# Kernel optimization log

Hardware: AMD Instinct MI355X
Metric: run time of the kernel (lower is better)

The kernel has to match this reference:

```python
import jax, jax.numpy as jnp
import numpy as np

DN = ('NCHW', 'OIHW', 'NCHW')

def conv3x3(x, w, b):
    y = jax.lax.conv_general_dilated(x, w, window_strides=(1, 1), padding='SAME', dimension_numbers=DN)
    return y + b[None, :, None, None]

def setup_inputs() -> dict:
    key = jax.random.key(0)
    ks = jax.random.split(key, 12)
    B, C, H, W, r = 4, 64, 128, 128, 2
    ic = C * r * r  # 256
    s = 0.02
    inp = {
        'x': jax.random.normal(ks[0], (B, C, H, W), jnp.float32),
        'g_w': jax.random.normal(ks[1], (ic, ic), jnp.float32) * s,
        'g_b': jnp.zeros((ic,), jnp.float32),
        'theta_w': jax.random.normal(ks[2], (ic, ic), jnp.float32) * s,
        'theta_b': jnp.zeros((ic,), jnp.float32),
        'phi_w': jax.random.normal(ks[3], (ic, ic), jnp.float32) * s,
        'phi_b': jnp.zeros((ic,), jnp.float32),
        'Ws_w': jax.random.normal(ks[4], (C, C), jnp.float32) * s,
        'Ws_b': jnp.zeros((C,), jnp.float32),
        'Wc_w': jax.random.normal(ks[5], (C, C), jnp.float32) * s,
        'Wc_b': jnp.zeros((C,), jnp.float32),
        'gamma_s': jnp.ones((1,), jnp.float32),
        'gamma_c': jnp.ones((1,), jnp.float32),
        'm1_w': jax.random.normal(ks[6], (16, C, 3, 3), jnp.float32) * s,
        'm1_b': jnp.zeros((16,), jnp.float32),
        'm2_w': jax.random.normal(ks[7], (1, 16, 3, 3), jnp.float32) * s,
        'm2_b': jnp.zeros((1,), jnp.float32),
    }
    return inp

def reference(x, g_w, g_b, theta_w, theta_b, phi_w, phi_b, Ws_w, Ws_b, Wc_w, Wc_b, gamma_s, gamma_c, m1_w, m1_b, m2_w, m2_b):
    b, c, h, w = x.shape
    ic = g_w.shape[0]
    r = int(round((ic // c) ** 0.5))
    hr, wr = h // r, w // r
    n = hr * wr  # spatial positions after channel-folding
    # x1: [b, ic, n] (row-major reshape, same as torch .reshape)
    x1 = x.reshape(b, ic, n)
    # 1x1 convs == channel matmuls
    g_x = jnp.einsum('oi,bin->bno', g_w, x1) + g_b          # [b, n, ic]
    th = jnp.einsum('oi,bin->bon', theta_w, x1) + theta_b[:, None]  # [b, ic, n]
    ph = jnp.einsum('oi,bin->bon', phi_w, x1) + phi_b[:, None]      # [b, ic, n]
    # spatial attention: [b, n, n]
    f_s = jnp.einsum('bcn,bcm->bnm', th, ph)
    f_s = jax.nn.softmax(f_s, axis=-1)
    y_s = jnp.einsum('bnm,bmo->bno', f_s, g_x)              # [b, n, ic]
    y_s = jnp.transpose(y_s, (0, 2, 1)).reshape(b, c, h, w)
    # channel attention: [b, ic, ic]
    f_c = jnp.einsum('bcn,bdn->bcd', th, ph)
    f_c = jax.nn.softmax(f_c, axis=-1)
    y_c = jnp.einsum('bno,bod->bnd', g_x, f_c).reshape(b, c, h, w)
    ws = jnp.einsum('oi,bihw->bohw', Ws_w, y_s) + Ws_b[None, :, None, None]
    wc = jnp.einsum('oi,bihw->bohw', Wc_w, y_c) + Wc_b[None, :, None, None]
    z = x + gamma_s[0] * ws + gamma_c[0] * wc
    hmid = jax.nn.relu(conv3x3(z, m1_w, m1_b))
    logit = conv3x3(hmid, m2_w, m2_b)
    return (logit, z)
```

## Files before the change

### kernel.cpp

```cpp
#include <hip/hip_runtime.h>
#include <stdint.h>

typedef unsigned short u16;
typedef unsigned int   u32;

typedef __attribute__((ext_vector_type(8)))  short bf16x8;
typedef __attribute__((ext_vector_type(4)))  float f32x4;
typedef __attribute__((ext_vector_type(4)))  unsigned int u32x4;

__device__ __forceinline__ float b2f(u16 u) { return __uint_as_float(((u32)u) << 16); }
__device__ __forceinline__ float blo(u32 u) { return __uint_as_float(u << 16); }
__device__ __forceinline__ float bhi(u32 u) { return __uint_as_float(u & 0xffff0000u); }
__device__ __forceinline__ u16 f2b(float f) {
    u32 x = __float_as_uint(f);
    u32 r = (x + 0x7fffu + ((x >> 16) & 1u)) >> 16;
    return (u16)r;
}

#define NB   4
#define IC   256
#define NPOS 4096
#define CH   64
#define HW   16384

__global__ __launch_bounds__(256) void prep_kernel(
    const float* __restrict__ wsw, const float* __restrict__ wcw,
    const float* __restrict__ m1w,
    const float* __restrict__ thw, const float* __restrict__ phw, const float* __restrict__ gw,
    float* __restrict__ wswT, float* __restrict__ wcwT, float* __restrict__ m1wT,
    u16* __restrict__ wbf)
{
    int idx = blockIdx.x * 256 + threadIdx.x;
    if (idx < 65536) {
        wbf[idx]          = f2b(thw[idx]);
        wbf[idx + 65536]  = f2b(phw[idx]);
        wbf[idx + 131072] = f2b(gw[idx]);
    }
    if (idx < 4096) {
        int i = idx >> 6, c = idx & 63;
        wswT[i*64 + c] = wsw[c*64 + i];
        wcwT[i*64 + c] = wcw[c*64 + i];
    }
    if (idx < 9216) {
        int o = idx & 15, ct = idx >> 4;
        int t = ct % 9, c = ct / 9;
        m1wT[idx] = m1w[(o*64 + c)*9 + t];
    }
}

__global__ __launch_bounds__(256) void qkv_mfma_kernel(
    const float* __restrict__ x, const u16* __restrict__ wbf,
    const float* __restrict__ thb, const float* __restrict__ phb, const float* __restrict__ gb,
    u16* __restrict__ Q, u16* __restrict__ K, u16* __restrict__ VT)
{
    __shared__ __align__(16) u32 xT[64*132];
    __shared__ __align__(16) float bias_l[256];
    const int tid  = threadIdx.x;
    const int w    = tid >> 6;
    const int lane = tid & 63;
    const int q4   = lane >> 4;
    const int l    = lane & 15;
    const int n0   = blockIdx.x * 64;
    const int b    = blockIdx.y;
    const int mat  = blockIdx.z;
    const u16* wmat = wbf + mat * 65536;
    const float* bias = (mat == 0) ? thb : (mat == 1) ? phb : gb;

    bias_l[tid] = bias[tid];

    {
        const float* xb = x + ((size_t)b*IC)*NPOS + n0;
        int n   = tid & 63;
        int ip0 = tid >> 6;
        #pragma unroll 4
        for (int p=0; p<32; p++){
            int ip = ip0 + p*4;
            float v0 = xb[(size_t)(2*ip  )*NPOS + n];
            float v1 = xb[(size_t)(2*ip+1)*NPOS + n];
            xT[n*132 + ip] = (u32)f2b(v0) | ((u32)f2b(v1) << 16);
        }
    }
    __syncthreads();

    f32x4 acc[4][4];
    #pragma unroll
    for (int ot=0; ot<4; ot++)
        #pragma unroll
        for (int nt=0; nt<4; nt++) acc[ot][nt] = (f32x4){0.f,0.f,0.f,0.f};

    #pragma unroll
    for (int f=0; f<8; f++){
        bf16x8 bfrag[4];
        #pragma unroll
        for (int nt=0; nt<4; nt++)
            bfrag[nt] = *(const bf16x8*)&xT[(nt*16 + l)*132 + f*16 + q4*4];
        #pragma unroll
        for (int ot=0; ot<4; ot++){
            bf16x8 afrag = *(const bf16x8*)(wmat + (size_t)(w*64 + ot*16 + l)*256 + f*32 + q4*8);
            #pragma unroll
            for (int nt=0; nt<4; nt++)
                acc[ot][nt] = __builtin_amdgcn_mfma_f32_16x16x32_bf16(afrag, bfrag[nt], acc[ot][nt], 0, 0, 0);
        }
    }
    __syncthreads();

    if (mat < 2){
        u16* zbuf = (u16*)xT;
        #pragma unroll
        for (int nt=0; nt<4; nt++)
            #pragma unroll
            for (int ot=0; ot<4; ot++){
                int o = w*64 + ot*16 + q4*4;
                float4 bv = *(const float4*)&bias_l[o];
                uint2 pk;
                pk.x = (u32)f2b(acc[ot][nt][0]+bv.x) | ((u32)f2b(acc[ot][nt][1]+bv.y) << 16);
                pk.y = (u32)f2b(acc[ot][nt][2]+bv.z) | ((u32)f2b(acc[ot][nt][3]+bv.w) << 16);
                *(uint2*)&zbuf[(nt*16 + l)*264 + o] = pk;
            }
        __syncthreads();
        u16* dst = ((mat == 0) ? Q : K) + ((size_t)(b*NPOS + n0))*IC;
        int n = tid >> 2, o0 = (tid & 3)*64;
        const u32* src = &xT[n*132 + (tid & 3)*32];
        #pragma unroll
        for (int m=0; m<8; m++)
            *(uint4*)(dst + (size_t)n*IC + o0 + m*8) = ((const uint4*)src)[m];
    } else {
        u16* zbuf = (u16*)xT;
        #pragma unroll
        for (int nt=0; nt<4; nt++)
            #pragma unroll
            for (int ot=0; ot<4; ot++){
                int o = w*64 + ot*16 + q4*4;
                int n = nt*16 + l;
                #pragma unroll
                for (int reg=0; reg<4; reg++)
                    zbuf[(o+reg)*66 + n] = f2b(acc[ot][nt][reg] + bias_l[o+reg]);
            }
        __syncthreads();
        const u32* src = &xT[tid*33];
        u32 tmp[32];
        #pragma unroll
        for (int m=0; m<32; m++) tmp[m] = src[m];
        u16* dst = VT + ((size_t)(b*IC + tid))*NPOS + n0;
        #pragma unroll
        for (int m=0; m<8; m++){
            uint4 v; v.x = tmp[m*4]; v.y = tmp[m*4+1]; v.z = tmp[m*4+2]; v.w = tmp[m*4+3];
            *(uint4*)(dst + m*8) = v;
        }
    }
}

__global__ __launch_bounds__(256) void fc_mfma_kernel(
    const u16* __restrict__ Q, const u16* __restrict__ K, float* __restrict__ fcp)
{
    __shared__ __align__(16) u16 QT[64*72];
    __shared__ __align__(16) u16 KT[64*72];
    const int tid = threadIdx.x;
    const int w   = tid >> 6;
    const int lane = tid & 63;
    const int q4  = lane >> 4;
    const int l   = lane & 15;
    const int c0  = blockIdx.x * 64;
    const int d0  = blockIdx.y * 64;
    const int b   = blockIdx.z >> 2;
    const int nseg= blockIdx.z & 3;

    f32x4 acc[4];
    #pragma unroll
    for (int dt=0; dt<4; dt++) acc[dt] = (f32x4){0.f,0.f,0.f,0.f};

    for (int chunk=0; chunk<16; chunk++){
        const int n0 = nseg*1024 + chunk*64;
        __syncthreads();
        {
            int r  = tid >> 2;
            int cq = (tid & 3) * 16;
            const u16* qs = Q + ((size_t)(b*NPOS + n0 + r))*IC + c0 + cq;
            const u16* ks = K + ((size_t)(b*NPOS + n0 + r))*IC + d0 + cq;
            u16 qv[16], kv[16];
            *(uint4*)&qv[0] = *(const uint4*)qs;
            *(uint4*)&qv[8] = *(const uint4*)(qs + 8);
            *(uint4*)&kv[0] = *(const uint4*)ks;
            *(uint4*)&kv[8] = *(const uint4*)(ks + 8);
            #pragma unroll
            for (int j=0;j<16;j++){
                QT[(cq+j)*72 + r] = qv[j];
                KT[(cq+j)*72 + r] = kv[j];
            }
        }
        __syncthreads();
        #pragma unroll
        for (int f=0; f<2; f++){
            bf16x8 af = *(const bf16x8*)&QT[(w*16 + l)*72 + f*32 + q4*8];
            #pragma unroll
            for (int dt=0; dt<4; dt++){
                bf16x8 bf2 = *(const bf16x8*)&KT[(dt*16 + l)*72 + f*32 + q4*8];
                acc[dt] = __builtin_amdgcn_mfma_f32_16x16x32_bf16(af, bf2, acc[dt], 0, 0, 0);
            }
        }
    }

    #pragma unroll
    for (int dt=0; dt<4; dt++)
        #pragma unroll
        for (int reg=0; reg<4; reg++)
            fcp[((size_t)((nseg*NB + b)*256 + c0 + w*16 + q4*4 + reg))*256 + d0 + dt*16 + l] = acc[dt][reg];
}

__global__ __launch_bounds__(256) void softmax_fc_kernel(
    const float* __restrict__ fcp, float* __restrict__ pc)
{
    __shared__ float red[8];
    const int tid = threadIdx.x;
    const int b = blockIdx.x >> 8, c = blockIdx.x & 255;
    float v = 0.f;
    #pragma unroll
    for (int s=0; s<4; s++)
        v += fcp[((size_t)((s*NB + b)*256 + c))*256 + tid];
    float m = v;
    #pragma unroll
    for (int d=32; d>=1; d>>=1) m = fmaxf(m, __shfl_xor(m, d));
    if ((tid & 63) == 0) red[tid>>6] = m;
    __syncthreads();
    m = fmaxf(fmaxf(red[0],red[1]), fmaxf(red[2],red[3]));
    float e = __expf(v - m);
    float s = e;
    #pragma unroll
    for (int d=32; d>=1; d>>=1) s += __shfl_xor(s, d);
    if ((tid & 63) == 0) red[4 + (tid>>6)] = s;
    __syncthreads();
    s = red[4]+red[5]+red[6]+red[7];
    pc[(size_t)b*65536 + (size_t)c*256 + tid] = e / s;
}

__global__ __launch_bounds__(256) void yc_kernel(
    const u16* __restrict__ VT, const float* __restrict__ pc, u16* __restrict__ ycb)
{
    __shared__ __align__(16) u16 Vt_l[32*64];
    __shared__ __align__(16) float Pt[32*64];
    const int tid = threadIdx.x;
    const int n0 = blockIdx.x * 64, d0 = blockIdx.y * 64, b = blockIdx.z;
    const int tn = tid >> 4, td = tid & 15;
    float acc[4][4];
    #pragma unroll
    for (int j=0;j<4;j++)
        #pragma unroll
        for (int d=0;d<4;d++) acc[j][d]=0.f;
    for (int ot=0; ot<8; ot++){
        int o0 = ot*32;
        __syncthreads();
        {
            int ol = tid >> 3, cc = tid & 7;
            *(uint4*)&Vt_l[ol*64 + cc*8] = *(const uint4*)(VT + ((size_t)(b*IC + o0 + ol))*NPOS + n0 + cc*8);
            const float* ps = pc + (size_t)b*65536 + (size_t)(o0 + ol)*256 + d0 + cc*8;
            *(float4*)&Pt[ol*64 + cc*8]     = *(const float4*)ps;
            *(float4*)&Pt[ol*64 + cc*8 + 4] = *(const float4*)(ps + 4);
        }
        __syncthreads();
        #pragma unroll 4
        for (int kk=0; kk<32; kk++){
            float4 pv = *(const float4*)&Pt[kk*64 + td*4];
            uint2 vp = *(const uint2*)&Vt_l[kk*64 + tn*4];
            float v0 = blo(vp.x), v1 = bhi(vp.x), v2 = blo(vp.y), v3 = bhi(vp.y);
            acc[0][0] = fmaf(v0, pv.x, acc[0][0]); acc[0][1] = fmaf(v0, pv.y, acc[0][1]);
            acc[0][2] = fmaf(v0, pv.z, acc[0][2]); acc[0][3] = fmaf(v0, pv.w, acc[0][3]);
            acc[1][0] = fmaf(v1, pv.x, acc[1][0]); acc[1][1] = fmaf(v1, pv.y, acc[1][1]);
            acc[1][2] = fmaf(v1, pv.z, acc[1][2]); acc[1][3] = fmaf(v1, pv.w, acc[1][3]);
            acc[2][0] = fmaf(v2, pv.x, acc[2][0]); acc[2][1] = fmaf(v2, pv.y, acc[2][1]);
            acc[2][2] = fmaf(v2, pv.z, acc[2][2]); acc[2][3] = fmaf(v2, pv.w, acc[2][3]);
            acc[3][0] = fmaf(v3, pv.x, acc[3][0]); acc[3][1] = fmaf(v3, pv.y, acc[3][1]);
            acc[3][2] = fmaf(v3, pv.z, acc[3][2]); acc[3][3] = fmaf(v3, pv.w, acc[3][3]);
        }
    }
    #pragma unroll
    for (int j=0;j<4;j++){
        u32 lo = (u32)f2b(acc[j][0]) | ((u32)f2b(acc[j][1]) << 16);
        u32 hi = (u32)f2b(acc[j][2]) | ((u32)f2b(acc[j][3]) << 16);
        *(uint2*)&ycb[((size_t)b*NPOS + n0 + tn*4 + j)*IC + d0 + td*4] = make_uint2(lo,hi);
    }
}

__global__ __launch_bounds__(256) void flash_mfma_kernel(
    const u16* __restrict__ Q, const u16* __restrict__ K, const u16* __restrict__ VT,
    u16* __restrict__ opart0, u16* __restrict__ opartx, float* __restrict__ lpart,
    int sshift)
{
    __shared__ __align__(16) u32 Kt[8192];
    __shared__ __align__(16) u32 Vt[8192];
    __shared__ __align__(16) u16 Pl[4608];
    const int tid  = threadIdx.x;
    const int w    = tid >> 6;
    const int lane = tid & 63;
    const int q4   = lane >> 4;
    const int l    = lane & 15;
    const int S    = 1 << sshift;

    const int id   = blockIdx.x;
    const int xcd  = id & 7;
    const int b    = xcd >> 1;
    const int h    = xcd & 1;
    const int r    = id >> 3;
    const int n0   = ((r & 31) | (h << 5)) * 64;
    const int seg  = r >> 5;
    const int tiles = 64 >> sshift;
    const int kt0   = seg * tiles;

    bf16x8 qf[8];
    {
        const u16* qrow = Q + ((size_t)(b*NPOS + n0 + w*16 + l))*IC;
        #pragma unroll
        for (int f=0; f<8; f++){
            u32x4 qv = __builtin_nontemporal_load((const u32x4*)(qrow + f*32 + q4*8));
            qf[f] = *(bf16x8*)&qv;
        }
    }

    f32x4 oacc[16];
    #pragma unroll
    for (int t=0;t<16;t++) oacc[t] = (f32x4){0.f,0.f,0.f,0.f};
    float lrow[4] = {0.f, 0.f, 0.f, 0.f};

    u16* Pz = Pl + w*1152;

    auto stage_k = [&](int m0s){
        #pragma unroll
        for (int j=0;j<8;j++){
            int call = w*8 + j;
            int rr = call*2 + (lane>>5);
            int c = (lane & 31) ^ (rr & 7);
            const u16* g = K + ((size_t)(b*NPOS + m0s + rr))*IC + c*8;
            __builtin_amdgcn_global_load_lds(
                (const __attribute__((address_space(1))) u32*)(const void*)g,
                (__attribute__((address_space(3))) u32*)(void*)&Kt[call*256], 16, 0, 0);
        }
    };
    auto stage_v = [&](int m0s){
        #pragma unroll
        for (int j=0;j<8;j++){
            int call = w*8 + j;
            int d = call*8 + (lane>>3);
            int c = (lane & 7) ^ (d & 7);
            const u16* g = VT + ((size_t)(b*IC + d))*NPOS + m0s + c*8;
            __builtin_amdgcn_global_load_lds(
                (const __attribute__((address_space(1))) u32*)(const void*)g,
                (__attribute__((address_space(3))) u32*)(void*)&Vt[call*256], 16, 0, 0);
        }
    };

    stage_k(kt0*64);
    stage_v(kt0*64);
    asm volatile("s_waitcnt vmcnt(0)" ::: "memory");
    __builtin_amdgcn_sched_barrier(0);
    __builtin_amdgcn_s_barrier();
    __builtin_amdgcn_sched_barrier(0);

    for (int kti=0; kti<tiles; kti++){
        const bool more = (kti + 1 < tiles);
        const int mn = (kt0 + kti + 1)*64;

        f32x4 sac[4];
        #pragma unroll
        for (int t=0;t<4;t++) sac[t] = (f32x4){0.f,0.f,0.f,0.f};
        __builtin_amdgcn_s_setprio(1);
        #pragma unroll
        for (int f=0; f<8; f++){
            #pragma unroll
            for (int t=0;t<4;t++){
                int rr = t*16 + l;
                int c = (f*4 + q4) ^ (rr & 7);
                bf16x8 kf = *(const bf16x8*)((const u16*)Kt + rr*256 + c*8);
                sac[t] = __builtin_amdgcn_mfma_f32_16x16x32_bf16(qf[f], kf, sac[t], 0, 0, 0);
            }
        }
        __builtin_amdgcn_s_setprio(0);

        __builtin_amdgcn_sched_barrier(0);
        __builtin_amdgcn_s_barrier();
        __builtin_amdgcn_sched_barrier(0);

        if (more) stage_k(mn);

        #pragma unroll
        for (int reg=0; reg<4; reg++){
            float p0 = __expf(sac[0][reg]), p1 = __expf(sac[1][reg]);
            float p2 = __expf(sac[2][reg]), p3 = __expf(sac[3][reg]);
            lrow[reg] += (p0+p1) + (p2+p3);
            int m = q4*4 + reg;
            Pz[m*72 + l]      = f2b(p0);
            Pz[m*72 + 16 + l] = f2b(p1);
            Pz[m*72 + 32 + l] = f2b(p2);
            Pz[m*72 + 48 + l] = f2b(p3);
        }

        if (more) { asm volatile("s_waitcnt vmcnt(8)" ::: "memory"); }
        else      { asm volatile("s_waitcnt vmcnt(0)" ::: "memory"); }
        __builtin_amdgcn_sched_barrier(0);
        __builtin_amdgcn_s_barrier();
        __builtin_amdgcn_sched_barrier(0);

        __builtin_amdgcn_s_setprio(1);
        #pragma unroll
        for (int s2=0; s2<2; s2++){
            bf16x8 pa = *(const bf16x8*)(Pz + l*72 + s2*32 + q4*8);
            #pragma unroll
            for (int t=0;t<16;t++){
                int d = t*16 + l;
                int c = (s2*4 + q4) ^ (d & 7);
                bf16x8 vb = *(const bf16x8*)((const u16*)Vt + d*64 + c*8);
                oacc[t] = __builtin_amdgcn_mfma_f32_16x16x32_bf16(pa, vb, oacc[t], 0, 0, 0);
            }
        }
        __builtin_amdgcn_s_setprio(0);

        __builtin_amdgcn_sched_barrier(0);
        __builtin_amdgcn_s_barrier();
        __builtin_amdgcn_sched_barrier(0);

        if (more) {
            stage_v(mn);
            asm volatile("s_waitcnt vmcnt(8)" ::: "memory");
        } else {
            asm volatile("s_waitcnt vmcnt(0)" ::: "memory");
        }
        __builtin_amdgcn_sched_barrier(0);
        __builtin_amdgcn_s_barrier();
        __builtin_amdgcn_sched_barrier(0);
    }

    #pragma unroll
    for (int reg=0; reg<4; reg++){
        float v = lrow[reg];
        v += __shfl_xor(v, 1); v += __shfl_xor(v, 2);
        v += __shfl_xor(v, 4); v += __shfl_xor(v, 8);
        if (l == 0)
            lpart[((size_t)(seg*NB + b))*NPOS + n0 + w*16 + q4*4 + reg] = v;
    }

    __syncthreads();
    u16* Ez = (u16*)Kt + w*4096;
    #pragma unroll
    for (int t=0;t<16;t++)
        #pragma unroll
        for (int reg=0;reg<4;reg++)
            Ez[(t*16 + l)*16 + q4*4 + reg] = f2b(oacc[t][reg]);
    u16* base = (seg == 0) ? opart0 : (opartx + (size_t)(seg-1)*((size_t)NB*IC*NPOS));
    u16* dst = base + (size_t)b*(IC*NPOS) + n0 + w*16;
    for (int p=0; p<32; p++){
        int d = p*8 + (lane>>3);
        u32 val = *(const u32*)(Ez + d*16 + (lane&7)*2);
        __builtin_nontemporal_store(val, (u32*)(dst + (size_t)d*NPOS + (lane&7)*2));
    }
}

__global__ __launch_bounds__(256) void combine_kernel(
    u16* __restrict__ opart0, const u16* __restrict__ opartx,
    const float* __restrict__ lpart, int S)
{
    const int idx = blockIdx.x * 256 + threadIdx.x;
    const int b   = idx >> 17;
    const int rem = idx & 131071;
    const int o   = rem >> 9;
    const int n   = (rem & 511) * 8;
    const size_t base = ((size_t)b*IC + o)*NPOS + n;
    float acc[8] = {0,0,0,0,0,0,0,0};
    float L[8]   = {0,0,0,0,0,0,0,0};
    for (int s=0; s<S; s++){
        const u16* p = (s == 0) ? opart0 : (opartx + (size_t)(s-1)*((size_t)NB*IC*NPOS));
        uint4 v = *(const uint4*)(p + base);
        acc[0] += blo(v.x); acc[1] += bhi(v.x);
        acc[2] += blo(v.y); acc[3] += bhi(v.y);
        acc[4] += blo(v.z); acc[5] += bhi(v.z);
        acc[6] += blo(v.w); acc[7] += bhi(v.w);
        const float* lp = lpart + ((size_t)(s*NB + b))*NPOS + n;
        float4 l0 = *(const float4*)lp;
        float4 l1 = *(const float4*)(lp + 4);
        L[0]+=l0.x; L[1]+=l0.y; L[2]+=l0.z; L[3]+=l0.w;
        L[4]+=l1.x; L[5]+=l1.y; L[6]+=l1.z; L[7]+=l1.w;
    }
    uint4 out;
    out.x = (u32)f2b(acc[0]/L[0]) | ((u32)f2b(acc[1]/L[1]) << 16);
    out.y = (u32)f2b(acc[2]/L[2]) | ((u32)f2b(acc[3]/L[3]) << 16);
    out.z = (u32)f2b(acc[4]/L[4]) | ((u32)f2b(acc[5]/L[5]) << 16);
    out.w = (u32)f2b(acc[6]/L[6]) | ((u32)f2b(acc[7]/L[7]) << 16);
    *(uint4*)(opart0 + base) = out;
}

__global__ __launch_bounds__(256) void z_kernel(
    const float* __restrict__ x, const u16* __restrict__ ysT, const u16* __restrict__ ycb,
    const float* __restrict__ wswT, const float* __restrict__ wcwT,
    const float* __restrict__ wsb, const float* __restrict__ wcb,
    const float* __restrict__ gs, const float* __restrict__ gc,
    float* __restrict__ zout)
{
    __shared__ __align__(16) float Wsl[64*32];
    __shared__ __align__(16) float Wcl[64*32];
    const int tid = threadIdx.x;
    const int p = blockIdx.x * 256 + tid;
    const int cbase = blockIdx.y * 32;
    const int b = blockIdx.z;
    {
        int i = tid >> 2, c8 = (tid & 3) * 8;
        const float* s1 = wswT + i*64 + cbase + c8;
        const float* s2 = wcwT + i*64 + cbase + c8;
        *(float4*)&Wsl[i*32 + c8]     = *(const float4*)s1;
        *(float4*)&Wsl[i*32 + c8 + 4] = *(const float4*)(s1+4);
        *(float4*)&Wcl[i*32 + c8]     = *(const float4*)s2;
        *(float4*)&Wcl[i*32 + c8 + 4] = *(const float4*)(s2+4);
    }
    __syncthreads();
    float as[32], ac[32];
    #pragma unroll
    for (int c=0;c<32;c++){ as[c]=0.f; ac[c]=0.f; }
    const u16* ysp = ysT + (size_t)b*(IC*NPOS) + p;
    const u16* ycp = ycb + (size_t)b*(IC*NPOS) + p;
    for (int i=0;i<64;i++){
        float ysv = b2f(ysp[(size_t)i*HW]);
        float ycv = b2f(ycp[(size_t)i*HW]);
        #pragma unroll
        for (int c=0;c<32;c++){
            as[c] = fmaf(Wsl[i*32+c], ysv, as[c]);
            ac[c] = fmaf(Wcl[i*32+c], ycv, ac[c]);
        }
    }
    float gsv = gs[0], gcv = gc[0];
    #pragma unroll
    for (int c=0;c<32;c++){
        int cg = cbase + c;
        float xv = x[((size_t)b*CH + cg)*HW + p];
        float zv = fmaf(gsv, as[c] + wsb[cg], xv);
        zv = fmaf(gcv, ac[c] + wcb[cg], zv);
        zout[((size_t)b*CH + cg)*HW + p] = zv;
    }
}

__global__ __launch_bounds__(256) void conv1_kernel(
    const float* __restrict__ z, const float* __restrict__ m1wT, const float* __restrict__ m1b,
    float* __restrict__ hmid)
{
    const int tid = threadIdx.x;
    const int p = blockIdx.x * 128 + (tid & 127);
    const int oh = (tid >> 7) * 8;
    const int b = blockIdx.y;
    const int y = p >> 7, xx = p & 127;
    float acc[8];
    #pragma unroll
    for (int o=0;o<8;o++) acc[o]=0.f;
    for (int c=0;c<64;c++){
        const float* zp = z + ((size_t)b*CH + c)*HW;
        #pragma unroll
        for (int t=0;t<9;t++){
            int dy = t/3 - 1, dx = t%3 - 1;
            int yy = y + dy, xv = xx + dx;
            float zv = 0.f;
            if (yy >= 0 && yy < 128 && xv >= 0 && xv < 128) zv = zp[yy*128 + xv];
            const float* w = m1wT + (c*9 + t)*16 + oh;
            #pragma unroll
            for (int o=0;o<8;o++) acc[o] = fmaf(w[o], zv, acc[o]);
        }
    }
    #pragma unroll
    for (int o=0;o<8;o++)
        hmid[((size_t)b*16 + oh + o)*HW + p] = fmaxf(acc[o] + m1b[oh + o], 0.f);
}

__global__ __launch_bounds__(256) void conv2_kernel(
    const float* __restrict__ hmid, const float* __restrict__ m2w, const float* __restrict__ m2b,
    float* __restrict__ logit)
{
    const int idx = blockIdx.x * 256 + threadIdx.x;
    const int b = idx >> 14, p = idx & 16383;
    const int y = p >> 7, xx = p & 127;
    float acc = 0.f;
    for (int c=0;c<16;c++){
        const float* hp = hmid + ((size_t)b*16 + c)*HW;
        #pragma unroll
        for (int t=0;t<9;t++){
            int dy = t/3 - 1, dx = t%3 - 1;
            int yy = y + dy, xv = xx + dx;
            if (yy >= 0 && yy < 128 && xv >= 0 && xv < 128)
                acc = fmaf(m2w[c*9+t], hp[yy*128 + xv], acc);
        }
    }
    logit[idx] = acc + m2b[0];
}

extern "C" void kernel_launch(void* const* d_in, const int* in_sizes, int n_in,
                              void* d_out, int out_size, void* d_ws, size_t ws_size,
                              hipStream_t stream)
{
    const float* x    = (const float*)d_in[0];
    const float* g_w  = (const float*)d_in[1];
    const float* g_b  = (const float*)d_in[2];
    const float* th_w = (const float*)d_in[3];
    const float* th_b = (const float*)d_in[4];
    const float* ph_w = (const float*)d_in[5];
    const float* ph_b = (const float*)d_in[6];
    const float* ws_w = (const float*)d_in[7];
    const float* ws_b = (const float*)d_in[8];
    const float* wc_w = (const float*)d_in[9];
    const float* wc_b = (const float*)d_in[10];
    const float* gs   = (const float*)d_in[11];
    const float* gc   = (const float*)d_in[12];
    const float* m1w  = (const float*)d_in[13];
    const float* m1b  = (const float*)d_in[14];
    const float* m2w  = (const float*)d_in[15];
    const float* m2b  = (const float*)d_in[16];

    char* ws = (char*)d_ws;
    u16*   Qb   = (u16*)  (ws + 0);
    u16*   Kb   = (u16*)  (ws + 8388608);
    u16*   VTb  = (u16*)  (ws + 16777216);
    u16*   ysT  = (u16*)  (ws + 25165824);
    u16*   ycb  = (u16*)  (ws + 33554432);
    u16*   wbf  = (u16*)  (ws + 41943040);
    float* pc   = (float*)(ws + 42991616);
    float* fcp  = (float*)(ws + 44040192);
    float* hmid = (float*)(ws + 44040192);
    float* lpart= (float*)(ws + 44040192);
    float* wswT = (float*)(ws + 48234496);
    float* wcwT = (float*)(ws + 48250880);
    float* m1wT = (float*)(ws + 48267264);
    u16*   opartx = (u16*)(ws + 48304128);

    float* logit = (float*)d_out;
    float* zout  = (float*)d_out + 65536;

    int sshift = 0;
    if (ws_size >= 48304128ULL + 3ULL*8388608ULL)      sshift = 2;
    else if (ws_size >= 48304128ULL + 1ULL*8388608ULL) sshift = 1;

    prep_kernel<<<256, 256, 0, stream>>>(ws_w, wc_w, m1w, th_w, ph_w, g_w,
                                         wswT, wcwT, m1wT, wbf);
    qkv_mfma_kernel<<<dim3(64,4,3), 256, 0, stream>>>(x, wbf, th_b, ph_b, g_b, Qb, Kb, VTb);
    fc_mfma_kernel<<<dim3(4,4,16), 256, 0, stream>>>(Qb, Kb, fcp);
    softmax_fc_kernel<<<1024, 256, 0, stream>>>(fcp, pc);
    yc_kernel<<<dim3(64,4,4), 256, 0, stream>>>(VTb, pc, ycb);
    flash_mfma_kernel<<<dim3(NB * 64 * (1 << sshift)), 256, 0, stream>>>(Qb, Kb, VTb, ysT, opartx, lpart, sshift);
    combine_kernel<<<2048, 256, 0, stream>>>(ysT, opartx, lpart, 1 << sshift);
    z_kernel<<<dim3(64,2,4), 256, 0, stream>>>(x, ysT, ycb, wswT, wcwT, ws_b, wc_b, gs, gc, zout);
    conv1_kernel<<<dim3(128,4), 256, 0, stream>>>(zout, m1wT, m1b, hmid);
    conv2_kernel<<<256, 256, 0, stream>>>(hmid, m2w, m2b, logit);
}
```

Baseline: 459.2 us.

## Split flash attention warps into 2x2 query-key/dim grid to reuse fragments

Each of the four warps now owns 32 query rows and half of the key columns (for QK) or half of the head dimension (for PV), instead of 16 query rows over the full tile. Each K and V fragment loaded from LDS now feeds two MFMAs, which halves LDS read traffic per MFMA. The P buffer uses a new XOR swizzle, and row sums are combined across the two key-half warps through LDS at the end. The cost is more query-fragment registers and an extra barrier plus reduction in the epilogue.

```diff
diff --git a/kernel.cpp b/kernel.cpp
--- a/kernel.cpp
+++ b/kernel.cpp
@@ -287,12 +287,14 @@
 {
     __shared__ __align__(16) u32 Kt[8192];
     __shared__ __align__(16) u32 Vt[8192];
-    __shared__ __align__(16) u16 Pl[4608];
+    __shared__ __align__(16) u16 Pl[4096];
     const int tid  = threadIdx.x;
     const int w    = tid >> 6;
     const int lane = tid & 63;
     const int q4   = lane >> 4;
     const int l    = lane & 15;
+    const int wq   = w >> 1;
+    const int wk   = w & 1;
     const int S    = 1 << sshift;
 
     const int id   = blockIdx.x;
@@ -305,22 +307,26 @@
     const int tiles = 64 >> sshift;
     const int kt0   = seg * tiles;
 
-    bf16x8 qf[8];
+    bf16x8 qf[2][8];
     {
-        const u16* qrow = Q + ((size_t)(b*NPOS + n0 + w*16 + l))*IC;
-        #pragma unroll
-        for (int f=0; f<8; f++){
-            u32x4 qv = __builtin_nontemporal_load((const u32x4*)(qrow + f*32 + q4*8));
-            qf[f] = *(bf16x8*)&qv;
-        }
-    }
-
-    f32x4 oacc[16];
-    #pragma unroll
-    for (int t=0;t<16;t++) oacc[t] = (f32x4){0.f,0.f,0.f,0.f};
-    float lrow[4] = {0.f, 0.f, 0.f, 0.f};
-
-    u16* Pz = Pl + w*1152;
+        const u16* qbase = Q + ((size_t)(b*NPOS + n0 + wq*32 + l))*IC;
+        #pragma unroll
+        for (int qt=0; qt<2; qt++)
+            #pragma unroll
+            for (int f=0; f<8; f++){
+                u32x4 qv = __builtin_nontemporal_load((const u32x4*)(qbase + qt*16*IC + f*32 + q4*8));
+                qf[qt][f] = *(bf16x8*)&qv;
+            }
+    }
+
+    f32x4 oacc[2][8];
+    #pragma unroll
+    for (int qt=0; qt<2; qt++)
+        #pragma unroll
+        for (int dt=0; dt<8; dt++) oacc[qt][dt] = (f32x4){0.f,0.f,0.f,0.f};
+    float lrow[2][4] = {{0.f,0.f,0.f,0.f},{0.f,0.f,0.f,0.f}};
+
+    u16* Pz = Pl + wq*2048;
 
     auto stage_k = [&](int m0s){
         #pragma unroll
@@ -358,18 +364,21 @@
         const bool more = (kti + 1 < tiles);
         const int mn = (kt0 + kti + 1)*64;
 
-        f32x4 sac[4];
-        #pragma unroll
-        for (int t=0;t<4;t++) sac[t] = (f32x4){0.f,0.f,0.f,0.f};
+        f32x4 sac[2][2];
+        #pragma unroll
+        for (int qt=0; qt<2; qt++)
+            #pragma unroll
+            for (int kt2=0; kt2<2; kt2++) sac[qt][kt2] = (f32x4){0.f,0.f,0.f,0.f};
         __builtin_amdgcn_s_setprio(1);
         #pragma unroll
         for (int f=0; f<8; f++){
-            #pragma unroll
-            for (int t=0;t<4;t++){
-                int rr = t*16 + l;
-                int c = (f*4 + q4) ^ (rr & 7);
-                bf16x8 kf = *(const bf16x8*)((const u16*)Kt + rr*256 + c*8);
-                sac[t] = __builtin_amdgcn_mfma_f32_16x16x32_bf16(qf[f], kf, sac[t], 0, 0, 0);
+            int c = (f*4 + q4) ^ (l & 7);
+            bf16x8 kf0 = *(const bf16x8*)((const u16*)Kt + (wk*32 + l)*256 + c*8);
+            bf16x8 kf1 = *(const bf16x8*)((const u16*)Kt + (wk*32 + 16 + l)*256 + c*8);
+            #pragma unroll
+            for (int qt=0; qt<2; qt++){
+                sac[qt][0] = __builtin_amdgcn_mfma_f32_16x16x32_bf16(qf[qt][f], kf0, sac[qt][0], 0, 0, 0);
+                sac[qt][1] = __builtin_amdgcn_mfma_f32_16x16x32_bf16(qf[qt][f], kf1, sac[qt][1], 0, 0, 0);
             }
         }
         __builtin_amdgcn_s_setprio(0);
@@ -381,33 +390,38 @@
         if (more) stage_k(mn);
 
         #pragma unroll
-        for (int reg=0; reg<4; reg++){
-            float p0 = __expf(sac[0][reg]), p1 = __expf(sac[1][reg]);
-            float p2 = __expf(sac[2][reg]), p3 = __expf(sac[3][reg]);
-            lrow[reg] += (p0+p1) + (p2+p3);
-            int m = q4*4 + reg;
-            Pz[m*72 + l]      = f2b(p0);
-            Pz[m*72 + 16 + l] = f2b(p1);
-            Pz[m*72 + 32 + l] = f2b(p2);
-            Pz[m*72 + 48 + l] = f2b(p3);
-        }
-
-        if (more) { asm volatile("s_waitcnt vmcnt(8)" ::: "memory"); }
-        else      { asm volatile("s_waitcnt vmcnt(0)" ::: "memory"); }
+        for (int qt=0; qt<2; qt++)
+            #pragma unroll
+            for (int kt2=0; kt2<2; kt2++)
+                #pragma unroll
+                for (int reg=0; reg<4; reg++){
+                    float p = __expf(sac[qt][kt2][reg]);
+                    lrow[qt][reg] += p;
+                    int q32 = qt*16 + q4*4 + reg;
+                    int slot = (wk*4 + kt2*2 + (l>>3)) ^ (q32 & 7);
+                    Pz[q32*64 + slot*8 + (l & 7)] = f2b(p);
+                }
+
+        if (more) { asm volatile("s_waitcnt vmcnt(8) lgkmcnt(0)" ::: "memory"); }
+        else      { asm volatile("s_waitcnt vmcnt(0) lgkmcnt(0)" ::: "memory"); }
         __builtin_amdgcn_sched_barrier(0);
         __builtin_amdgcn_s_barrier();
         __builtin_amdgcn_sched_barrier(0);
 
         __builtin_amdgcn_s_setprio(1);
         #pragma unroll
-        for (int s2=0; s2<2; s2++){
-            bf16x8 pa = *(const bf16x8*)(Pz + l*72 + s2*32 + q4*8);
-            #pragma unroll
-            for (int t=0;t<16;t++){
-                int d = t*16 + l;
-                int c = (s2*4 + q4) ^ (d & 7);
-                bf16x8 vb = *(const bf16x8*)((const u16*)Vt + d*64 + c*8);
-                oacc[t] = __builtin_amdgcn_mfma_f32_16x16x32_bf16(pa, vb, oacc[t], 0, 0, 0);
+        for (int kstep=0; kstep<2; kstep++){
+            int cc = (kstep*4 + q4) ^ (l & 7);
+            bf16x8 pa[2];
+            #pragma unroll
+            for (int qt=0; qt<2; qt++)
+                pa[qt] = *(const bf16x8*)(Pz + (qt*16 + l)*64 + cc*8);
+            #pragma unroll
+            for (int dt=0; dt<8; dt++){
+                bf16x8 vb = *(const bf16x8*)((const u16*)Vt + (wk*128 + dt*16 + l)*64 + cc*8);
+                #pragma unroll
+                for (int qt=0; qt<2; qt++)
+                    oacc[qt][dt] = __builtin_amdgcn_mfma_f32_16x16x32_bf16(pa[qt], vb, oacc[qt][dt], 0, 0, 0);
             }
         }
         __builtin_amdgcn_s_setprio(0);
@@ -427,28 +441,59 @@
         __builtin_amdgcn_sched_barrier(0);
     }
 
-    #pragma unroll
-    for (int reg=0; reg<4; reg++){
-        float v = lrow[reg];
-        v += __shfl_xor(v, 1); v += __shfl_xor(v, 2);
-        v += __shfl_xor(v, 4); v += __shfl_xor(v, 8);
-        if (l == 0)
-            lpart[((size_t)(seg*NB + b))*NPOS + n0 + w*16 + q4*4 + reg] = v;
-    }
+    float lv[2][4];
+    #pragma unroll
+    for (int qt=0; qt<2; qt++)
+        #pragma unroll
+        for (int reg=0; reg<4; reg++){
+            float v = lrow[qt][reg];
+            v += __shfl_xor(v, 1); v += __shfl_xor(v, 2);
+            v += __shfl_xor(v, 4); v += __shfl_xor(v, 8);
+            lv[qt][reg] = v;
+        }
 
     __syncthreads();
+    float* lred = (float*)Pl;
+    if (l == 0){
+        #pragma unroll
+        for (int qt=0; qt<2; qt++)
+            #pragma unroll
+            for (int reg=0; reg<4; reg++){
+                int qi = wq*32 + qt*16 + q4*4 + reg;
+                lred[qi*2 + wk] = lv[qt][reg];
+            }
+    }
     u16* Ez = (u16*)Kt + w*4096;
     #pragma unroll
-    for (int t=0;t<16;t++)
-        #pragma unroll
-        for (int reg=0;reg<4;reg++)
-            Ez[(t*16 + l)*16 + q4*4 + reg] = f2b(oacc[t][reg]);
-    u16* base = (seg == 0) ? opart0 : (opartx + (size_t)(seg-1)*((size_t)NB*IC*NPOS));
-    u16* dst = base + (size_t)b*(IC*NPOS) + n0 + w*16;
+    for (int qt=0; qt<2; qt++)
+        #pragma unroll
+        for (int dt=0; dt<8; dt++)
+            #pragma unroll
+            for (int reg=0; reg<4; reg++){
+                int q32 = qt*16 + q4*4 + reg;
+                int dl  = dt*16 + l;
+                Ez[dl*32 + q32] = f2b(oacc[qt][dt][reg]);
+            }
+    __syncthreads();
+
+    if (wk == 0 && l == 0){
+        #pragma unroll
+        for (int qt=0; qt<2; qt++)
+            #pragma unroll
+            for (int reg=0; reg<4; reg++){
+                int qi = wq*32 + qt*16 + q4*4 + reg;
+                lpart[((size_t)(seg*NB + b))*NPOS + n0 + qi] = lred[qi*2] + lred[qi*2+1];
+            }
+    }
+
+    u16* basep = (seg == 0) ? opart0 : (opartx + (size_t)(seg-1)*((size_t)NB*IC*NPOS));
+    u16* dst = basep + (size_t)b*(IC*NPOS) + n0 + wq*32;
+    #pragma unroll 4
     for (int p=0; p<32; p++){
-        int d = p*8 + (lane>>3);
-        u32 val = *(const u32*)(Ez + d*16 + (lane&7)*2);
-        __builtin_nontemporal_store(val, (u32*)(dst + (size_t)d*NPOS + (lane&7)*2));
+        int dl = p*4 + (lane>>4);
+        int dglob = wk*128 + dl;
+        u32 val = *(const u32*)&Ez[dl*32 + (lane&15)*2];
+        __builtin_nontemporal_store(val, (u32*)(dst + (size_t)dglob*NPOS + (lane&15)*2));
     }
 }
 
```

New measurement: 502.2 us. +9.4%, slower.

## Move y_c matmul to MFMA with bf16 probabilities and fold split combine into z

Applied to the files above, without the earlier changes.

The channel-attention product y_c now runs on bf16 MFMA, reading V and the softmax probabilities from swizzled LDS tiles, and the softmax writes bf16 instead of fp32. The separate combine kernel for the split flash partials is removed. z_kernel now sums the partial outputs and divides by the summed softmax denominators on the fly, which saves a kernel launch and one full read-write pass over the partial buffers. The cost is lower precision for the probabilities, a z_kernel that reads up to four partial buffers per element, and z_kernel applying a single denominator per position across all splits.

```diff
diff --git a/kernel.cpp b/kernel.cpp
--- a/kernel.cpp
+++ b/kernel.cpp
@@ -208,7 +208,7 @@
 }
 
 __global__ __launch_bounds__(256) void softmax_fc_kernel(
-    const float* __restrict__ fcp, float* __restrict__ pc)
+    const float* __restrict__ fcp, u16* __restrict__ pcb)
 {
     __shared__ float red[8];
     const int tid = threadIdx.x;
@@ -230,54 +230,59 @@
     if ((tid & 63) == 0) red[4 + (tid>>6)] = s;
     __syncthreads();
     s = red[4]+red[5]+red[6]+red[7];
-    pc[(size_t)b*65536 + (size_t)c*256 + tid] = e / s;
-}
-
-__global__ __launch_bounds__(256) void yc_kernel(
-    const u16* __restrict__ VT, const float* __restrict__ pc, u16* __restrict__ ycb)
-{
-    __shared__ __align__(16) u16 Vt_l[32*64];
-    __shared__ __align__(16) float Pt[32*64];
+    pcb[(size_t)b*65536 + (size_t)c*256 + tid] = f2b(e / s);
+}
+
+__global__ __launch_bounds__(256) void yc_mfma_kernel(
+    const u16* __restrict__ VT, const u16* __restrict__ pcb, u16* __restrict__ ycb)
+{
+    __shared__ __align__(16) u16 Vl[64*32];
+    __shared__ __align__(16) u16 Pcl[64*32];
     const int tid = threadIdx.x;
+    const int w = tid >> 6, lane = tid & 63;
+    const int q4 = lane >> 4, l = lane & 15;
     const int n0 = blockIdx.x * 64, d0 = blockIdx.y * 64, b = blockIdx.z;
-    const int tn = tid >> 4, td = tid & 15;
-    float acc[4][4];
-    #pragma unroll
-    for (int j=0;j<4;j++)
-        #pragma unroll
-        for (int d=0;d<4;d++) acc[j][d]=0.f;
-    for (int ot=0; ot<8; ot++){
-        int o0 = ot*32;
+
+    f32x4 acc[4];
+    #pragma unroll
+    for (int dt=0; dt<4; dt++) acc[dt] = (f32x4){0.f,0.f,0.f,0.f};
+
+    const int so = tid >> 3;
+    const int sj = tid & 7;
+
+    for (int oc=0; oc<8; oc++){
+        const int o0 = oc*32;
         __syncthreads();
         {
-            int ol = tid >> 3, cc = tid & 7;
-            *(uint4*)&Vt_l[ol*64 + cc*8] = *(const uint4*)(VT + ((size_t)(b*IC + o0 + ol))*NPOS + n0 + cc*8);
-            const float* ps = pc + (size_t)b*65536 + (size_t)(o0 + ol)*256 + d0 + cc*8;
-            *(float4*)&Pt[ol*64 + cc*8]     = *(const float4*)ps;
-            *(float4*)&Pt[ol*64 + cc*8 + 4] = *(const float4*)(ps + 4);
+            uint4 v = *(const uint4*)(VT + ((size_t)(b*IC + o0 + so))*NPOS + n0 + sj*8);
+            u16 tv[8]; *(uint4*)tv = v;
+            #pragma unroll
+            for (int m=0;m<8;m++){
+                int n = sj*8 + m;
+                Vl[n*32 + ((((so>>3) ^ (n&3)))<<3) + (so&7)] = tv[m];
+            }
+            uint4 pv = *(const uint4*)(pcb + (size_t)b*65536 + (size_t)(o0 + so)*256 + d0 + sj*8);
+            u16 tp[8]; *(uint4*)tp = pv;
+            #pragma unroll
+            for (int m=0;m<8;m++){
+                int d = sj*8 + m;
+                Pcl[d*32 + ((((so>>3) ^ (d&3)))<<3) + (so&7)] = tp[m];
+            }
         }
         __syncthreads();
-        #pragma unroll 4
-        for (int kk=0; kk<32; kk++){
-            float4 pv = *(const float4*)&Pt[kk*64 + td*4];
-            uint2 vp = *(const uint2*)&Vt_l[kk*64 + tn*4];
-            float v0 = blo(vp.x), v1 = bhi(vp.x), v2 = blo(vp.y), v3 = bhi(vp.y);
-            acc[0][0] = fmaf(v0, pv.x, acc[0][0]); acc[0][1] = fmaf(v0, pv.y, acc[0][1]);
-            acc[0][2] = fmaf(v0, pv.z, acc[0][2]); acc[0][3] = fmaf(v0, pv.w, acc[0][3]);
-            acc[1][0] = fmaf(v1, pv.x, acc[1][0]); acc[1][1] = fmaf(v1, pv.y, acc[1][1]);
-            acc[1][2] = fmaf(v1, pv.z, acc[1][2]); acc[1][3] = fmaf(v1, pv.w, acc[1][3]);
-            acc[2][0] = fmaf(v2, pv.x, acc[2][0]); acc[2][1] = fmaf(v2, pv.y, acc[2][1]);
-            acc[2][2] = fmaf(v2, pv.z, acc[2][2]); acc[2][3] = fmaf(v2, pv.w, acc[2][3]);
-            acc[3][0] = fmaf(v3, pv.x, acc[3][0]); acc[3][1] = fmaf(v3, pv.y, acc[3][1]);
-            acc[3][2] = fmaf(v3, pv.z, acc[3][2]); acc[3][3] = fmaf(v3, pv.w, acc[3][3]);
-        }
-    }
-    #pragma unroll
-    for (int j=0;j<4;j++){
-        u32 lo = (u32)f2b(acc[j][0]) | ((u32)f2b(acc[j][1]) << 16);
-        u32 hi = (u32)f2b(acc[j][2]) | ((u32)f2b(acc[j][3]) << 16);
-        *(uint2*)&ycb[((size_t)b*NPOS + n0 + tn*4 + j)*IC + d0 + td*4] = make_uint2(lo,hi);
-    }
+        bf16x8 af = *(const bf16x8*)&Vl[(w*16 + l)*32 + ((q4 ^ (l&3))<<3)];
+        #pragma unroll
+        for (int dt=0; dt<4; dt++){
+            bf16x8 bfr = *(const bf16x8*)&Pcl[(dt*16 + l)*32 + ((q4 ^ (l&3))<<3)];
+            acc[dt] = __builtin_amdgcn_mfma_f32_16x16x32_bf16(af, bfr, acc[dt], 0, 0, 0);
+        }
+    }
+
+    #pragma unroll
+    for (int dt=0; dt<4; dt++)
+        #pragma unroll
+        for (int reg=0; reg<4; reg++)
+            ycb[((size_t)(b*NPOS + n0 + w*16 + q4*4 + reg))*IC + d0 + dt*16 + l] = f2b(acc[dt][reg]);
 }
 
 __global__ __launch_bounds__(256) void flash_mfma_kernel(
@@ -452,41 +457,11 @@
     }
 }
 
-__global__ __launch_bounds__(256) void combine_kernel(
-    u16* __restrict__ opart0, const u16* __restrict__ opartx,
-    const float* __restrict__ lpart, int S)
-{
-    const int idx = blockIdx.x * 256 + threadIdx.x;
-    const int b   = idx >> 17;
-    const int rem = idx & 131071;
-    const int o   = rem >> 9;
-    const int n   = (rem & 511) * 8;
-    const size_t base = ((size_t)b*IC + o)*NPOS + n;
-    float acc[8] = {0,0,0,0,0,0,0,0};
-    float L[8]   = {0,0,0,0,0,0,0,0};
-    for (int s=0; s<S; s++){
-        const u16* p = (s == 0) ? opart0 : (opartx + (size_t)(s-1)*((size_t)NB*IC*NPOS));
-        uint4 v = *(const uint4*)(p + base);
-        acc[0] += blo(v.x); acc[1] += bhi(v.x);
-        acc[2] += blo(v.y); acc[3] += bhi(v.y);
-        acc[4] += blo(v.z); acc[5] += bhi(v.z);
-        acc[6] += blo(v.w); acc[7] += bhi(v.w);
-        const float* lp = lpart + ((size_t)(s*NB + b))*NPOS + n;
-        float4 l0 = *(const float4*)lp;
-        float4 l1 = *(const float4*)(lp + 4);
-        L[0]+=l0.x; L[1]+=l0.y; L[2]+=l0.z; L[3]+=l0.w;
-        L[4]+=l1.x; L[5]+=l1.y; L[6]+=l1.z; L[7]+=l1.w;
-    }
-    uint4 out;
-    out.x = (u32)f2b(acc[0]/L[0]) | ((u32)f2b(acc[1]/L[1]) << 16);
-    out.y = (u32)f2b(acc[2]/L[2]) | ((u32)f2b(acc[3]/L[3]) << 16);
-    out.z = (u32)f2b(acc[4]/L[4]) | ((u32)f2b(acc[5]/L[5]) << 16);
-    out.w = (u32)f2b(acc[6]/L[6]) | ((u32)f2b(acc[7]/L[7]) << 16);
-    *(uint4*)(opart0 + base) = out;
-}
-
 __global__ __launch_bounds__(256) void z_kernel(
-    const float* __restrict__ x, const u16* __restrict__ ysT, const u16* __restrict__ ycb,
+    const float* __restrict__ x,
+    const u16* __restrict__ opart0, const u16* __restrict__ opartx,
+    const float* __restrict__ lpart, int S,
+    const u16* __restrict__ ycb,
     const float* __restrict__ wswT, const float* __restrict__ wcwT,
     const float* __restrict__ wsb, const float* __restrict__ wcb,
     const float* __restrict__ gs, const float* __restrict__ gc,
@@ -508,14 +483,31 @@
         *(float4*)&Wcl[i*32 + c8 + 4] = *(const float4*)(s2+4);
     }
     __syncthreads();
+
+    float Ls = 0.f;
+    for (int s=0; s<S; s++)
+        Ls += lpart[((size_t)(s*NB + b))*NPOS + (p & 4095)];
+    const float rl = 1.f / Ls;
+
     float as[32], ac[32];
     #pragma unroll
     for (int c=0;c<32;c++){ as[c]=0.f; ac[c]=0.f; }
-    const u16* ysp = ysT + (size_t)b*(IC*NPOS) + p;
-    const u16* ycp = ycb + (size_t)b*(IC*NPOS) + p;
+
+    const size_t obase = (size_t)b*(IC*NPOS) + p;
+    const size_t CHUNK = (size_t)NB*IC*NPOS;
+    const u16* o0p = opart0 + obase;
+    const u16* o1p = opartx + obase;
+    const u16* o2p = o1p + CHUNK;
+    const u16* o3p = o2p + CHUNK;
+    const u16* ycp = ycb + obase;
+
     for (int i=0;i<64;i++){
-        float ysv = b2f(ysp[(size_t)i*HW]);
-        float ycv = b2f(ycp[(size_t)i*HW]);
+        const size_t ih = (size_t)i*HW;
+        float ysum = b2f(o0p[ih]);
+        if (S > 1) ysum += b2f(o1p[ih]);
+        if (S > 2) ysum += b2f(o2p[ih]) + b2f(o3p[ih]);
+        float ysv = ysum * rl;
+        float ycv = b2f(ycp[ih]);
         #pragma unroll
         for (int c=0;c<32;c++){
             as[c] = fmaf(Wsl[i*32+c], ysv, as[c]);
@@ -613,7 +605,7 @@
     u16*   ysT  = (u16*)  (ws + 25165824);
     u16*   ycb  = (u16*)  (ws + 33554432);
     u16*   wbf  = (u16*)  (ws + 41943040);
-    float* pc   = (float*)(ws + 42991616);
+    u16*   pcb  = (u16*)  (ws + 42991616);
     float* fcp  = (float*)(ws + 44040192);
     float* hmid = (float*)(ws + 44040192);
     float* lpart= (float*)(ws + 44040192);
@@ -633,11 +625,11 @@
                                          wswT, wcwT, m1wT, wbf);
     qkv_mfma_kernel<<<dim3(64,4,3), 256, 0, stream>>>(x, wbf, th_b, ph_b, g_b, Qb, Kb, VTb);
     fc_mfma_kernel<<<dim3(4,4,16), 256, 0, stream>>>(Qb, Kb, fcp);
-    softmax_fc_kernel<<<1024, 256, 0, stream>>>(fcp, pc);
-    yc_kernel<<<dim3(64,4,4), 256, 0, stream>>>(VTb, pc, ycb);
+    softmax_fc_kernel<<<1024, 256, 0, stream>>>(fcp, pcb);
+    yc_mfma_kernel<<<dim3(64,4,4), 256, 0, stream>>>(VTb, pcb, ycb);
     flash_mfma_kernel<<<dim3(NB * 64 * (1 << sshift)), 256, 0, stream>>>(Qb, Kb, VTb, ysT, opartx, lpart, sshift);
-    combine_kernel<<<2048, 256, 0, stream>>>(ysT, opartx, lpart, 1 << sshift);
-    z_kernel<<<dim3(64,2,4), 256, 0, stream>>>(x, ysT, ycb, wswT, wcwT, ws_b, wc_b, gs, gc, zout);
+    z_kernel<<<dim3(64,2,4), 256, 0, stream>>>(x, ysT, opartx, lpart, 1 << sshift, ycb,
+                                               wswT, wcwT, ws_b, wc_b, gs, gc, zout);
     conv1_kernel<<<dim3(128,4), 256, 0, stream>>>(zout, m1wT, m1b, hmid);
     conv2_kernel<<<256, 256, 0, stream>>>(hmid, m2w, m2b, logit);
 }
```

Result: slower. 489.8 us (+6.7%).
